# Kernel optimization log

Hardware: AMD Instinct MI355X
Metric: run time of the kernel (lower is better)

The kernel has to match this reference:

```python
import jax, jax.numpy as jnp
import numpy as np

NUM_LEVELS = 4
RADIUS = 4


def _avg_pool2(x):
    # x: [N, H, W] -> [N, H//2, W//2], 2x2 mean pool, stride 2 (F.avg_pool2d(corr,2,2))
    N, H, W = x.shape
    return x.reshape(N, H // 2, 2, W // 2, 2).mean(axis=(2, 4))


def _bilinear_sample(img, x, y):
    # img: [N, H, W]; x, y: [N, P] pixel coords.
    # Matches F.grid_sample(..., mode='bilinear', align_corners=True, padding_mode='zeros')
    # after the pixel->normalized->pixel round trip in bilinear_sampler (identity).
    N, H, W = img.shape
    x0 = jnp.floor(x)
    y0 = jnp.floor(y)
    wx = x - x0
    wy = y - y0
    x0i = x0.astype(jnp.int32)
    y0i = y0.astype(jnp.int32)
    flat = img.reshape(N, H * W)

    def gather(yi, xi):
        valid = (xi >= 0) & (xi <= W - 1) & (yi >= 0) & (yi <= H - 1)
        idx = jnp.clip(yi, 0, H - 1) * W + jnp.clip(xi, 0, W - 1)
        v = jnp.take_along_axis(flat, idx, axis=1)
        return jnp.where(valid, v, jnp.zeros((), img.dtype))

    v00 = gather(y0i, x0i)
    v01 = gather(y0i, x0i + 1)
    v10 = gather(y0i + 1, x0i)
    v11 = gather(y0i + 1, x0i + 1)
    return (v00 * (1 - wy) * (1 - wx) + v01 * (1 - wy) * wx
            + v10 * wy * (1 - wx) + v11 * wy * wx)


def _corr_block(fmap1, fmap2, coords):
    B, D, H, W = fmap1.shape
    # all-pairs correlation: [B, H*W, H*W] / sqrt(D)
    f1 = fmap1.reshape(B, D, H * W)
    f2 = fmap2.reshape(B, D, H * W)
    corr = jnp.einsum('bdn,bdm->bnm', f1, f2) / jnp.sqrt(jnp.asarray(D, fmap1.dtype))
    corr = corr.reshape(B * H * W, H, W)
    pyramid = [corr]
    for _ in range(NUM_LEVELS - 1):
        corr = _avg_pool2(corr)
        pyramid.append(corr)

    # coords: [B, 2, H, W] (x, y) -> [B*H*W, 2]
    c = coords.transpose(0, 2, 3, 1).reshape(B * H * W, 2)
    r = RADIUS
    d = jnp.linspace(-r, r, 2 * r + 1)
    dyg, dxg = jnp.meshgrid(d, d, indexing='ij')
    # faithful to torch: delta = stack(meshgrid(dy, dx), -1); channel 0 added to x, 1 to y
    delta = jnp.stack([dyg, dxg], axis=-1).reshape(-1, 2)  # [81, 2]

    outs = []
    for i, lvl in enumerate(pyramid):
        cl = c[:, None, :] / (2.0 ** i) + delta[None, :, :]  # [N, 81, 2]
        s = _bilinear_sample(lvl, cl[..., 0], cl[..., 1])    # [N, 81]
        outs.append(s.reshape(B, H, W, (2 * r + 1) ** 2))
    out = jnp.concatenate(outs, axis=-1)                     # [B, H, W, 4*81]
    return out.transpose(0, 3, 1, 2).astype(jnp.float32)


def setup_inputs() -> dict:
    key = jax.random.key(0)
    k1, k2, k3 = jax.random.split(key, 3)
    B, D, H, W = 2, 256, 80, 80
    fmap1 = jax.random.normal(k1, (B, D, H, W), dtype=jnp.float32)
    fmap2 = jax.random.normal(k2, (B, D, H, W), dtype=jnp.float32)
    # pixel coords in [0, W-1] x [0, H-1] (channel 0 = x, channel 1 = y)
    u = jax.random.uniform(k3, (B, 2, H, W), dtype=jnp.float32)
    scale = jnp.asarray([W - 1, H - 1], jnp.float32).reshape(1, 2, 1, 1)
    coords = u * scale
    return {"fmap1": fmap1, "fmap2": fmap2, "coords": coords}


def reference(fmap1, fmap2, coords):
    return _corr_block(fmap1, fmap2, coords)
```

## Files before the change

kernel.cpp:

```cpp
#include <hip/hip_runtime.h>


typedef _Float16 h2 __attribute__((ext_vector_type(2)));
typedef _Float16 half8 __attribute__((ext_vector_type(8)));
typedef float f32x4 __attribute__((ext_vector_type(4)));

#define HWDIM 80
#define DCH 256
#define NPIX 12800
#define NBUCKET 800

__global__ __launch_bounds__(256) void transpose_all(const float* __restrict__ f1,
                                                     const float* __restrict__ f2,
                                                     _Float16* __restrict__ f1h,
                                                     _Float16* __restrict__ f2p0) {
    __shared__ float tile[256][33];
    int bid = blockIdx.x;
    bool isf1 = bid < 400;
    int lb = isf1 ? bid : bid - 400;
    const float* src = isf1 ? f1 : f2;
    int b = lb / 200;
    int s0 = (lb % 200) * 32;
    int t = threadIdx.x;
    const float* sb = src + (size_t)b * DCH * (HWDIM * HWDIM);
#pragma unroll 4
    for (int k = 0; k < 32; ++k) {
        int j = t + 256 * k;
        int c = j >> 5, s = j & 31;
        tile[c][s] = sb[(size_t)c * (HWDIM * HWDIM) + s0 + s];
    }
    __syncthreads();
    int p = t & 127;
    int srow = t >> 7;
    if (isf1) {
        _Float16* db = f1h + ((size_t)b * 6400 + s0) * DCH;
#pragma unroll 4
        for (int k = 0; k < 16; ++k) {
            int s = 2 * k + srow;
            h2 v;
            v[0] = (_Float16)tile[2 * p][s];
            v[1] = (_Float16)tile[2 * p + 1][s];
            *(h2*)(db + (size_t)s * DCH + 2 * p) = v;
        }
    } else {
#pragma unroll 4
        for (int k = 0; k < 16; ++k) {
            int s = 2 * k + srow;
            int spatial = s0 + s;
            int yy = spatial / 80;
            int xx = spatial - yy * 80;
            h2 v;
            v[0] = (_Float16)tile[2 * p][s];
            v[1] = (_Float16)tile[2 * p + 1][s];
            size_t off = (size_t)b * 2073600 + (size_t)(p >> 4) * 259200
                       + ((size_t)(yy + 5) * 90 + (xx + 5)) * 32 + ((2 * p) & 31);
            *(h2*)(f2p0 + off) = v;
        }
    }
}

__global__ __launch_bounds__(256) void pool1(const _Float16* __restrict__ src,
                                             _Float16* __restrict__ dst) {
    int i = blockIdx.x * 256 + threadIdx.x;
    int c2 = i & 15;
    int r = i >> 4;
    int x = r % 40; r /= 40;
    int y = r % 40; r /= 40;
    int pl = r & 7;
    int b = r >> 3;
    const h2* s = (const h2*)src + ((size_t)b * 2073600 + (size_t)pl * 259200) / 2
                + ((size_t)(2 * y + 5) * 90 + (2 * x + 5)) * 16 + c2;
    h2 v00 = s[0], v01 = s[16], v10 = s[90 * 16], v11 = s[90 * 16 + 16];
    float r0 = ((float)v00[0] + (float)v01[0] + (float)v10[0] + (float)v11[0]) * 0.25f;
    float r1 = ((float)v00[1] + (float)v01[1] + (float)v10[1] + (float)v11[1]) * 0.25f;
    h2 o; o[0] = (_Float16)r0; o[1] = (_Float16)r1;
    *((h2*)dst + ((size_t)b * 640000 + (size_t)pl * 80000) / 2
      + ((size_t)(y + 5) * 50 + (x + 5)) * 16 + c2) = o;
}

__global__ __launch_bounds__(256) void pool23(const _Float16* __restrict__ l1,
                                              _Float16* __restrict__ l2,
                                              _Float16* __restrict__ l3) {
    int i = blockIdx.x * 256 + threadIdx.x;
    if (i < 102400) {
        int c2 = i & 15;
        int r = i >> 4;
        int x = r % 20; r /= 20;
        int y = r % 20; r /= 20;
        int pl = r & 7;
        int b = r >> 3;
        const h2* s = (const h2*)l1 + ((size_t)b * 640000 + (size_t)pl * 80000) / 2
                    + ((size_t)(2 * y + 5) * 50 + (2 * x + 5)) * 16 + c2;
        h2 v00 = s[0], v01 = s[16], v10 = s[50 * 16], v11 = s[50 * 16 + 16];
        float r0 = ((float)v00[0] + (float)v01[0] + (float)v10[0] + (float)v11[0]) * 0.25f;
        float r1 = ((float)v00[1] + (float)v01[1] + (float)v10[1] + (float)v11[1]) * 0.25f;
        h2 o; o[0] = (_Float16)r0; o[1] = (_Float16)r1;
        *((h2*)l2 + ((size_t)b * 230400 + (size_t)pl * 28800) / 2
          + ((size_t)(y + 5) * 30 + (x + 5)) * 16 + c2) = o;
    } else {
        int j = i - 102400;
        int c2 = j & 15;
        int r = j >> 4;
        int x = r % 10; r /= 10;
        int y = r % 10; r /= 10;
        int pl = r & 7;
        int b = r >> 3;
        const h2* s = (const h2*)l1 + ((size_t)b * 640000 + (size_t)pl * 80000) / 2 + c2;
        float r0 = 0.f, r1 = 0.f;
#pragma unroll
        for (int dy = 0; dy < 4; ++dy)
#pragma unroll
            for (int dx = 0; dx < 4; ++dx) {
                h2 v = s[((size_t)(4 * y + dy + 5) * 50 + (4 * x + dx + 5)) * 16];
                r0 += (float)v[0];
                r1 += (float)v[1];
            }
        h2 o; o[0] = (_Float16)(r0 * 0.0625f); o[1] = (_Float16)(r1 * 0.0625f);
        *((h2*)l3 + ((size_t)b * 102400 + (size_t)pl * 12800) / 2
          + ((size_t)(y + 5) * 20 + (x + 5)) * 16 + c2) = o;
    }
}

static __device__ __forceinline__ int bucket_of(const float* coords, int n) {
    int b = n / 6400;
    int r = n - b * 6400;
    float cx = coords[(size_t)b * 12800 + r];
    float cy = coords[(size_t)b * 12800 + 6400 + r];
    int ix = min(max((int)floorf(cx), 0), 79);
    int iy = min(max((int)floorf(cy), 0), 79);
    return b * 400 + (iy >> 2) * 20 + (ix >> 2);
}

__global__ __launch_bounds__(1024) void bucket_k(const float* __restrict__ coords,
                                                 int* __restrict__ sortedIdxP,
                                                 int* __restrict__ rank) {
    __shared__ unsigned int histS[NBUCKET], startS[NBUCKET], curS[NBUCKET];
    __shared__ unsigned int waveSum[16];
    int t = threadIdx.x;
    if (t < NBUCKET) histS[t] = 0u;
    __syncthreads();
    int bkt[13];
#pragma unroll
    for (int i = 0; i < 13; ++i) {
        int n = i * 1024 + t;
        if (n < NPIX) {
            bkt[i] = bucket_of(coords, n);
            atomicAdd(&histS[bkt[i]], 1u);
        }
    }
    __syncthreads();
    unsigned int v = (t < NBUCKET) ? ((histS[t] + 15u) & ~15u) : 0u;
    unsigned int x = v;
#pragma unroll
    for (int d = 1; d < 64; d <<= 1) {
        unsigned int y = __shfl_up(x, d);
        if ((t & 63) >= d) x += y;
    }
    if ((t & 63) == 63) waveSum[t >> 6] = x;
    __syncthreads();
    if (t < 16) {
        unsigned int w = waveSum[t];
#pragma unroll
        for (int d = 1; d < 16; d <<= 1) {
            unsigned int y = __shfl_up(w, d);
            if (t >= d) w += y;
        }
        waveSum[t] = w;
    }
    __syncthreads();
    unsigned int incl = x + ((t >> 6) ? waveSum[(t >> 6) - 1] : 0u);
    if (t < NBUCKET) {
        unsigned int e = incl - v;
        startS[t] = e;
        curS[t] = e;
    }
    __syncthreads();
#pragma unroll
    for (int i = 0; i < 13; ++i) {
        int n = i * 1024 + t;
        if (n < NPIX) {
            unsigned int pos = atomicAdd(&curS[bkt[i]], 1u);
            sortedIdxP[pos] = n;
            rank[n] = (int)pos;
        }
    }
    __syncthreads();
    if (t < NBUCKET) {
        unsigned int h = histS[t];
        if (h) {
            unsigned int pc = (h + 15u) & ~15u;
            unsigned int base = startS[t];
            int dup = sortedIdxP[base];
            for (unsigned int s = h; s < pc; ++s) sortedIdxP[base + s] = dup;
        }
    }
}

__global__ __launch_bounds__(512, 4) void corr_mfma(
    const _Float16* __restrict__ f1h,
    const _Float16* __restrict__ f2p0, const _Float16* __restrict__ f2p1,
    const _Float16* __restrict__ f2p2, const _Float16* __restrict__ f2p3,
    const float* __restrict__ coords, const int* __restrict__ sortedIdxP,
    _Float16* __restrict__ scratch) {
    __shared__ float G[528 * 17];
    __shared__ float fxS[4][16], fyS[4][16];
    __shared__ int lxS[4][16], lyS[4][16];
    __shared__ int X0cS[4], Y0cS[4], bS;

    int pphys = blockIdx.x;
    int l = (pphys & 7) * 200 + (pphys >> 3);
    int tid = threadIdx.x;
    if (sortedIdxP[l * 16] < 0) return;
    int lane = tid & 63;
    int wave = tid >> 6;

    int npx = sortedIdxP[l * 16 + (lane & 15)];
    const float4* f1p = (const float4*)(f1h + (size_t)npx * DCH);
    half8 bf[8];
#pragma unroll
    for (int kk = 0; kk < 8; ++kk)
        bf[kk] = __builtin_bit_cast(half8, f1p[(lane >> 4) + 4 * kk]);

    if (tid < 64) {
        int px = tid & 15, Lt = tid >> 4;
        int n = sortedIdxP[l * 16 + px];
        int b = n / 6400;
        int r = n - b * 6400;
        float cx = coords[(size_t)b * 12800 + r];
        float cy = coords[(size_t)b * 12800 + 6400 + r];
        float ls = 1.0f / (float)(1 << Lt);
        float cxl = cx * ls, cyl = cy * ls;
        float fxf = floorf(cxl), fyf = floorf(cyl);
        int X0 = (int)fxf - 4, Y0 = (int)fyf - 4;
        int ix = min(max((int)floorf(cx), 0), 79);
        int iy = min(max((int)floorf(cy), 0), 79);
        int X0c = (((ix >> 2) * 4) >> Lt) - 4;
        int Y0c = (((iy >> 2) * 4) >> Lt) - 4;
        lxS[Lt][px] = min(max(X0 - X0c, 0), 3);
        lyS[Lt][px] = min(max(Y0 - Y0c, 0), 3);
        fxS[Lt][px] = cxl - fxf;
        fyS[Lt][px] = cyl - fyf;
        X0cS[Lt] = X0c;
        Y0cS[Lt] = Y0c;
        if (tid == 0) bS = sortedIdxP[l * 16] / 6400;
    }
    __syncthreads();
    int b = bS;
    _Float16* sc = scratch + (size_t)l * 5184;

#pragma unroll
    for (int tt = 0; tt < 33; ++tt) {
        const int L  = tt < 11 ? 0 : tt < 19 ? 1 : tt < 26 ? 2 : 3;
        const int rt = tt - (L == 0 ? 0 : L == 1 ? 11 : L == 2 ? 19 : 26);
        const int Ww = L == 0 ? 13 : L == 1 ? 11 : 10;
        const int MT = L == 0 ? 169 : L == 1 ? 121 : 100;
        const int MAG = L == 0 ? 161320 : L == 1 ? 190652 : 209716;
        const int Wp = L == 0 ? 90 : L == 1 ? 50 : L == 2 ? 30 : 20;
        const int PS = L == 0 ? 259200 : L == 1 ? 80000 : L == 2 ? 28800 : 12800;
        const int PB = L == 0 ? 2073600 : L == 1 ? 640000 : L == 2 ? 230400 : 102400;
        const int GO = L == 0 ? 0 : L == 1 ? 176 : L == 2 ? 304 : 416;
        if (tt == 32 ? (wave != 7) : ((tt & 7) != wave)) continue;
        const _Float16* f2L = (L == 0 ? f2p0 : L == 1 ? f2p1 : L == 2 ? f2p2 : f2p3);
        const _Float16* f2b = f2L + (size_t)b * PB
                            + ((size_t)(Y0cS[L] + 5) * Wp + (X0cS[L] + 5)) * 32;
        int m = min(rt * 16 + (lane & 15), MT - 1);
        int my = (m * MAG) >> 21;
        int mx = m - my * Ww;
        const float4* ap = (const float4*)(f2b + (size_t)(my * Wp + mx) * 32)
                         + (lane >> 4);
        f32x4 acc = {0.f, 0.f, 0.f, 0.f};
#pragma unroll
        for (int kk = 0; kk < 8; ++kk) {
            half8 av = __builtin_bit_cast(half8, ap[kk * (PS / 8)]);
            acc = __builtin_amdgcn_mfma_f32_16x16x32_f16(av, bf[kk], acc, 0, 0, 0);
        }
        int gr = GO + rt * 16 + (lane >> 4) * 4;
#pragma unroll
        for (int r = 0; r < 4; ++r) G[(gr + r) * 17 + (lane & 15)] = acc[r];
    }
    __syncthreads();

    for (int idx = tid; idx < 5184; idx += 512) {
        int k2 = idx >> 4, x = idx & 15;
        int Le = (k2 * 810) >> 16;
        int k = k2 - Le * 81;
        int Ww = Le == 0 ? 13 : Le == 1 ? 11 : 10;
        int GO = Le == 0 ? 0 : Le == 1 ? 176 : Le == 2 ? 304 : 416;
        int a = (k * 57) >> 9;
        int c = k - 9 * a;
        int gx = lxS[Le][x] + a, gy = lyS[Le][x] + c;
        int m00 = GO + gy * Ww + gx;
        float fx = fxS[Le][x], fy = fyS[Le][x];
        float t00 = G[m00 * 17 + x];
        float t01 = G[(m00 + 1) * 17 + x];
        float t10 = G[(m00 + Ww) * 17 + x];
        float t11 = G[(m00 + Ww + 1) * 17 + x];
        float v = ((1.f - fy) * ((1.f - fx) * t00 + fx * t01)
                 + fy * ((1.f - fx) * t10 + fx * t11)) * 0.0625f;
        sc[idx] = (_Float16)v;
    }
}

__global__ __launch_bounds__(256) void unsort4(const _Float16* __restrict__ scratch,
                                               const int* __restrict__ rank,
                                               float* __restrict__ out) {
    int u = blockIdx.x * 256 + threadIdx.x;
    int q = u % 1600;
    int ch = (u / 1600) % 324;
    int b = u / (1600 * 324);
    int nl = q * 4;
    int4 rk = *(const int4*)(rank + b * 6400 + nl);
    float4 v;
    v.x = (float)scratch[(size_t)(rk.x >> 4) * 5184 + ch * 16 + (rk.x & 15)];
    v.y = (float)scratch[(size_t)(rk.y >> 4) * 5184 + ch * 16 + (rk.y & 15)];
    v.z = (float)scratch[(size_t)(rk.z >> 4) * 5184 + ch * 16 + (rk.z & 15)];
    v.w = (float)scratch[(size_t)(rk.w >> 4) * 5184 + ch * 16 + (rk.w & 15)];
    *(float4*)(out + ((size_t)b * 324 + ch) * 6400 + nl) = v;
}

extern "C" void kernel_launch(void* const* d_in, const int* in_sizes, int n_in,
                              void* d_out, int out_size, void* d_ws, size_t ws_size,
                              hipStream_t stream) {
    const float* fmap1 = (const float*)d_in[0];
    const float* fmap2 = (const float*)d_in[1];
    const float* coords = (const float*)d_in[2];
    float* out = (float*)d_out;
    char* ws = (char*)d_ws;

    _Float16* f1h  = (_Float16*)(ws);
    _Float16* f2p0 = (_Float16*)(ws + 6553600);
    _Float16* f2p1 = (_Float16*)(ws + 14848000);
    _Float16* f2p2 = (_Float16*)(ws + 17408000);
    _Float16* f2p3 = (_Float16*)(ws + 18329600);
    int* sortedIdxP = (int*)(ws + 18739200);
    int* rank       = (int*)(ws + 18841600);
    _Float16* scratch = (_Float16*)(ws + 18892800);

    hipMemsetAsync(f2p0, 0, 12185600, stream);
    hipMemsetAsync(sortedIdxP, 0xFF, 102400, stream);

    transpose_all<<<dim3(800), dim3(256), 0, stream>>>(fmap1, fmap2, f1h, f2p0);
    pool1<<<dim3(1600), dim3(256), 0, stream>>>(f2p0, f2p1);
    pool23<<<dim3(500), dim3(256), 0, stream>>>(f2p1, f2p2, f2p3);
    bucket_k<<<dim3(1), dim3(1024), 0, stream>>>(coords, sortedIdxP, rank);
    corr_mfma<<<dim3(1600), dim3(512), 0, stream>>>(f1h, f2p0, f2p1, f2p2, f2p3,
                                                    coords, sortedIdxP, scratch);
    unsort4<<<dim3(4050), dim3(256), 0, stream>>>(scratch, rank, out);
}
```

Measured before the change: 104.3 us.

## Fuse pooling kernels, drop memset, stage f1 in LDS, rebalance MFMA tiles

Merges the two pooling kernels into one launch that computes all three coarser levels directly from level 0, so later levels no longer wait on earlier ones. The memset of the sorted index buffer is removed; the bucket kernel now writes -1 into its unused tail. In the correlation kernel, f1 feature vectors are loaded once into LDS with coalesced loads, and the 33 tiles are split into contiguous compile-time ranges per wave. Launch bounds drop to 2 blocks, which frees registers but may reduce occupancy, and pooling straight from level 0 does more reads per output.

```diff
diff --git a/kernel.cpp b/kernel.cpp
--- a/kernel.cpp
+++ b/kernel.cpp
@@ -59,64 +59,67 @@
     }
 }
 
-__global__ __launch_bounds__(256) void pool1(const _Float16* __restrict__ src,
-                                             _Float16* __restrict__ dst) {
+__global__ __launch_bounds__(256) void pools(const _Float16* __restrict__ l0,
+                                             _Float16* __restrict__ l1,
+                                             _Float16* __restrict__ l2,
+                                             _Float16* __restrict__ l3) {
     int i = blockIdx.x * 256 + threadIdx.x;
-    int c2 = i & 15;
-    int r = i >> 4;
-    int x = r % 40; r /= 40;
-    int y = r % 40; r /= 40;
-    int pl = r & 7;
-    int b = r >> 3;
-    const h2* s = (const h2*)src + ((size_t)b * 2073600 + (size_t)pl * 259200) / 2
-                + ((size_t)(2 * y + 5) * 90 + (2 * x + 5)) * 16 + c2;
-    h2 v00 = s[0], v01 = s[16], v10 = s[90 * 16], v11 = s[90 * 16 + 16];
-    float r0 = ((float)v00[0] + (float)v01[0] + (float)v10[0] + (float)v11[0]) * 0.25f;
-    float r1 = ((float)v00[1] + (float)v01[1] + (float)v10[1] + (float)v11[1]) * 0.25f;
-    h2 o; o[0] = (_Float16)r0; o[1] = (_Float16)r1;
-    *((h2*)dst + ((size_t)b * 640000 + (size_t)pl * 80000) / 2
-      + ((size_t)(y + 5) * 50 + (x + 5)) * 16 + c2) = o;
-}
-
-__global__ __launch_bounds__(256) void pool23(const _Float16* __restrict__ l1,
-                                              _Float16* __restrict__ l2,
-                                              _Float16* __restrict__ l3) {
-    int i = blockIdx.x * 256 + threadIdx.x;
-    if (i < 102400) {
+    if (i < 409600) {
         int c2 = i & 15;
         int r = i >> 4;
+        int x = r % 40; r /= 40;
+        int y = r % 40; r /= 40;
+        int pl = r & 7;
+        int b = r >> 3;
+        const h2* s = (const h2*)l0 + (size_t)b * 1036800 + (size_t)pl * 129600
+                    + ((size_t)(2 * y + 5) * 90 + (2 * x + 5)) * 16 + c2;
+        h2 v00 = s[0], v01 = s[16], v10 = s[90 * 16], v11 = s[90 * 16 + 16];
+        float r0 = ((float)v00[0] + (float)v01[0] + (float)v10[0] + (float)v11[0]) * 0.25f;
+        float r1 = ((float)v00[1] + (float)v01[1] + (float)v10[1] + (float)v11[1]) * 0.25f;
+        h2 o; o[0] = (_Float16)r0; o[1] = (_Float16)r1;
+        *((h2*)l1 + (size_t)b * 320000 + (size_t)pl * 40000
+          + ((size_t)(y + 5) * 50 + (x + 5)) * 16 + c2) = o;
+    } else if (i < 512000) {
+        int j = i - 409600;
+        int c2 = j & 15;
+        int r = j >> 4;
         int x = r % 20; r /= 20;
         int y = r % 20; r /= 20;
         int pl = r & 7;
         int b = r >> 3;
-        const h2* s = (const h2*)l1 + ((size_t)b * 640000 + (size_t)pl * 80000) / 2
-                    + ((size_t)(2 * y + 5) * 50 + (2 * x + 5)) * 16 + c2;
-        h2 v00 = s[0], v01 = s[16], v10 = s[50 * 16], v11 = s[50 * 16 + 16];
-        float r0 = ((float)v00[0] + (float)v01[0] + (float)v10[0] + (float)v11[0]) * 0.25f;
-        float r1 = ((float)v00[1] + (float)v01[1] + (float)v10[1] + (float)v11[1]) * 0.25f;
-        h2 o; o[0] = (_Float16)r0; o[1] = (_Float16)r1;
-        *((h2*)l2 + ((size_t)b * 230400 + (size_t)pl * 28800) / 2
+        const h2* s = (const h2*)l0 + (size_t)b * 1036800 + (size_t)pl * 129600 + c2;
+        float r0 = 0.f, r1 = 0.f;
+#pragma unroll
+        for (int dy = 0; dy < 4; ++dy)
+#pragma unroll
+            for (int dx = 0; dx < 4; ++dx) {
+                h2 v = s[((size_t)(4 * y + dy + 5) * 90 + (4 * x + dx + 5)) * 16];
+                r0 += (float)v[0];
+                r1 += (float)v[1];
+            }
+        h2 o; o[0] = (_Float16)(r0 * 0.0625f); o[1] = (_Float16)(r1 * 0.0625f);
+        *((h2*)l2 + (size_t)b * 115200 + (size_t)pl * 14400
           + ((size_t)(y + 5) * 30 + (x + 5)) * 16 + c2) = o;
     } else {
-        int j = i - 102400;
+        int j = i - 512000;
         int c2 = j & 15;
         int r = j >> 4;
         int x = r % 10; r /= 10;
         int y = r % 10; r /= 10;
         int pl = r & 7;
         int b = r >> 3;
-        const h2* s = (const h2*)l1 + ((size_t)b * 640000 + (size_t)pl * 80000) / 2 + c2;
+        const h2* s = (const h2*)l0 + (size_t)b * 1036800 + (size_t)pl * 129600 + c2;
         float r0 = 0.f, r1 = 0.f;
 #pragma unroll
-        for (int dy = 0; dy < 4; ++dy)
-#pragma unroll
-            for (int dx = 0; dx < 4; ++dx) {
-                h2 v = s[((size_t)(4 * y + dy + 5) * 50 + (4 * x + dx + 5)) * 16];
+        for (int dy = 0; dy < 8; ++dy)
+#pragma unroll
+            for (int dx = 0; dx < 8; ++dx) {
+                h2 v = s[((size_t)(8 * y + dy + 5) * 90 + (8 * x + dx + 5)) * 16];
                 r0 += (float)v[0];
                 r1 += (float)v[1];
             }
-        h2 o; o[0] = (_Float16)(r0 * 0.0625f); o[1] = (_Float16)(r1 * 0.0625f);
-        *((h2*)l3 + ((size_t)b * 102400 + (size_t)pl * 12800) / 2
+        h2 o; o[0] = (_Float16)(r0 * 0.015625f); o[1] = (_Float16)(r1 * 0.015625f);
+        *((h2*)l3 + (size_t)b * 51200 + (size_t)pl * 6400
           + ((size_t)(y + 5) * 20 + (x + 5)) * 16 + c2) = o;
     }
 }
@@ -136,6 +139,7 @@
                                                  int* __restrict__ rank) {
     __shared__ unsigned int histS[NBUCKET], startS[NBUCKET], curS[NBUCKET];
     __shared__ unsigned int waveSum[16];
+    __shared__ unsigned int totalS;
     int t = threadIdx.x;
     if (t < NBUCKET) histS[t] = 0u;
     __syncthreads();
@@ -173,6 +177,7 @@
         unsigned int e = incl - v;
         startS[t] = e;
         curS[t] = e;
+        if (t == NBUCKET - 1) totalS = incl;
     }
     __syncthreads();
 #pragma unroll
@@ -194,15 +199,54 @@
             for (unsigned int s = h; s < pc; ++s) sortedIdxP[base + s] = dup;
         }
     }
-}
-
-__global__ __launch_bounds__(512, 4) void corr_mfma(
+    for (unsigned int s = totalS + t; s < 25600u; s += 1024u) sortedIdxP[s] = -1;
+}
+
+template <int TB, int TE>
+static __device__ __forceinline__ void run_tiles(
+    int lane, int b,
+    const _Float16* __restrict__ f2p0, const _Float16* __restrict__ f2p1,
+    const _Float16* __restrict__ f2p2, const _Float16* __restrict__ f2p3,
+    const int* X0cS, const int* Y0cS, const half8* bf, float* G) {
+#pragma unroll
+    for (int tt = TB; tt < TE; ++tt) {
+        const int L  = tt < 11 ? 0 : tt < 19 ? 1 : tt < 26 ? 2 : 3;
+        const int rt = tt - (L == 0 ? 0 : L == 1 ? 11 : L == 2 ? 19 : 26);
+        const int Ww = L == 0 ? 13 : L == 1 ? 11 : 10;
+        const int MT = L == 0 ? 169 : L == 1 ? 121 : 100;
+        const int MAG = L == 0 ? 161320 : L == 1 ? 190652 : 209716;
+        const int Wp = L == 0 ? 90 : L == 1 ? 50 : L == 2 ? 30 : 20;
+        const int PS = L == 0 ? 259200 : L == 1 ? 80000 : L == 2 ? 28800 : 12800;
+        const int PB = L == 0 ? 2073600 : L == 1 ? 640000 : L == 2 ? 230400 : 102400;
+        const int GO = L == 0 ? 0 : L == 1 ? 176 : L == 2 ? 304 : 416;
+        const _Float16* f2L = (L == 0 ? f2p0 : L == 1 ? f2p1 : L == 2 ? f2p2 : f2p3);
+        const _Float16* f2b = f2L + (size_t)b * PB
+                            + ((size_t)(Y0cS[L] + 5) * Wp + (X0cS[L] + 5)) * 32;
+        int m = min(rt * 16 + (lane & 15), MT - 1);
+        int my = (m * MAG) >> 21;
+        int mx = m - my * Ww;
+        const float4* ap = (const float4*)(f2b + (size_t)(my * Wp + mx) * 32)
+                         + (lane >> 4);
+        f32x4 acc = {0.f, 0.f, 0.f, 0.f};
+#pragma unroll
+        for (int kk = 0; kk < 8; ++kk) {
+            half8 av = __builtin_bit_cast(half8, ap[kk * (PS / 8)]);
+            acc = __builtin_amdgcn_mfma_f32_16x16x32_f16(av, bf[kk], acc, 0, 0, 0);
+        }
+        int gr = GO + rt * 16 + (lane >> 4) * 4;
+#pragma unroll
+        for (int r = 0; r < 4; ++r) G[(gr + r) * 17 + (lane & 15)] = acc[r];
+    }
+}
+
+__global__ __launch_bounds__(512, 2) void corr_mfma(
     const _Float16* __restrict__ f1h,
     const _Float16* __restrict__ f2p0, const _Float16* __restrict__ f2p1,
     const _Float16* __restrict__ f2p2, const _Float16* __restrict__ f2p3,
     const float* __restrict__ coords, const int* __restrict__ sortedIdxP,
     _Float16* __restrict__ scratch) {
     __shared__ float G[528 * 17];
+    __shared__ _Float16 f1S[16 * 264];
     __shared__ float fxS[4][16], fyS[4][16];
     __shared__ int lxS[4][16], lyS[4][16];
     __shared__ int X0cS[4], Y0cS[4], bS;
@@ -214,13 +258,12 @@
     int lane = tid & 63;
     int wave = tid >> 6;
 
-    int npx = sortedIdxP[l * 16 + (lane & 15)];
-    const float4* f1p = (const float4*)(f1h + (size_t)npx * DCH);
-    half8 bf[8];
-#pragma unroll
-    for (int kk = 0; kk < 8; ++kk)
-        bf[kk] = __builtin_bit_cast(half8, f1p[(lane >> 4) + 4 * kk]);
-
+    {
+        int px = tid >> 5, q = tid & 31;
+        int n = sortedIdxP[l * 16 + px];
+        const float4* src = (const float4*)(f1h + (size_t)n * DCH);
+        *((float4*)(f1S + px * 264) + q) = src[q];
+    }
     if (tid < 64) {
         int px = tid & 15, Lt = tid >> 4;
         int n = sortedIdxP[l * 16 + px];
@@ -246,40 +289,23 @@
     }
     __syncthreads();
     int b = bS;
+
+    half8 bf[8];
+#pragma unroll
+    for (int kk = 0; kk < 8; ++kk)
+        bf[kk] = *(const half8*)(f1S + (lane & 15) * 264 + ((lane >> 4) + 4 * kk) * 8);
+
+    if      (wave == 0) run_tiles<0, 5>(lane, b, f2p0, f2p1, f2p2, f2p3, X0cS, Y0cS, bf, G);
+    else if (wave == 1) run_tiles<5, 9>(lane, b, f2p0, f2p1, f2p2, f2p3, X0cS, Y0cS, bf, G);
+    else if (wave == 2) run_tiles<9, 13>(lane, b, f2p0, f2p1, f2p2, f2p3, X0cS, Y0cS, bf, G);
+    else if (wave == 3) run_tiles<13, 17>(lane, b, f2p0, f2p1, f2p2, f2p3, X0cS, Y0cS, bf, G);
+    else if (wave == 4) run_tiles<17, 21>(lane, b, f2p0, f2p1, f2p2, f2p3, X0cS, Y0cS, bf, G);
+    else if (wave == 5) run_tiles<21, 25>(lane, b, f2p0, f2p1, f2p2, f2p3, X0cS, Y0cS, bf, G);
+    else if (wave == 6) run_tiles<25, 29>(lane, b, f2p0, f2p1, f2p2, f2p3, X0cS, Y0cS, bf, G);
+    else                run_tiles<29, 33>(lane, b, f2p0, f2p1, f2p2, f2p3, X0cS, Y0cS, bf, G);
+    __syncthreads();
+
     _Float16* sc = scratch + (size_t)l * 5184;
-
-#pragma unroll
-    for (int tt = 0; tt < 33; ++tt) {
-        const int L  = tt < 11 ? 0 : tt < 19 ? 1 : tt < 26 ? 2 : 3;
-        const int rt = tt - (L == 0 ? 0 : L == 1 ? 11 : L == 2 ? 19 : 26);
-        const int Ww = L == 0 ? 13 : L == 1 ? 11 : 10;
-        const int MT = L == 0 ? 169 : L == 1 ? 121 : 100;
-        const int MAG = L == 0 ? 161320 : L == 1 ? 190652 : 209716;
-        const int Wp = L == 0 ? 90 : L == 1 ? 50 : L == 2 ? 30 : 20;
-        const int PS = L == 0 ? 259200 : L == 1 ? 80000 : L == 2 ? 28800 : 12800;
-        const int PB = L == 0 ? 2073600 : L == 1 ? 640000 : L == 2 ? 230400 : 102400;
-        const int GO = L == 0 ? 0 : L == 1 ? 176 : L == 2 ? 304 : 416;
-        if (tt == 32 ? (wave != 7) : ((tt & 7) != wave)) continue;
-        const _Float16* f2L = (L == 0 ? f2p0 : L == 1 ? f2p1 : L == 2 ? f2p2 : f2p3);
-        const _Float16* f2b = f2L + (size_t)b * PB
-                            + ((size_t)(Y0cS[L] + 5) * Wp + (X0cS[L] + 5)) * 32;
-        int m = min(rt * 16 + (lane & 15), MT - 1);
-        int my = (m * MAG) >> 21;
-        int mx = m - my * Ww;
-        const float4* ap = (const float4*)(f2b + (size_t)(my * Wp + mx) * 32)
-                         + (lane >> 4);
-        f32x4 acc = {0.f, 0.f, 0.f, 0.f};
-#pragma unroll
-        for (int kk = 0; kk < 8; ++kk) {
-            half8 av = __builtin_bit_cast(half8, ap[kk * (PS / 8)]);
-            acc = __builtin_amdgcn_mfma_f32_16x16x32_f16(av, bf[kk], acc, 0, 0, 0);
-        }
-        int gr = GO + rt * 16 + (lane >> 4) * 4;
-#pragma unroll
-        for (int r = 0; r < 4; ++r) G[(gr + r) * 17 + (lane & 15)] = acc[r];
-    }
-    __syncthreads();
-
     for (int idx = tid; idx < 5184; idx += 512) {
         int k2 = idx >> 4, x = idx & 15;
         int Le = (k2 * 810) >> 16;
@@ -337,11 +363,9 @@
     _Float16* scratch = (_Float16*)(ws + 18892800);
 
     hipMemsetAsync(f2p0, 0, 12185600, stream);
-    hipMemsetAsync(sortedIdxP, 0xFF, 102400, stream);
 
     transpose_all<<<dim3(800), dim3(256), 0, stream>>>(fmap1, fmap2, f1h, f2p0);
-    pool1<<<dim3(1600), dim3(256), 0, stream>>>(f2p0, f2p1);
-    pool23<<<dim3(500), dim3(256), 0, stream>>>(f2p1, f2p2, f2p3);
+    pools<<<dim3(2100), dim3(256), 0, stream>>>(f2p0, f2p1, f2p2, f2p3);
     bucket_k<<<dim3(1), dim3(1024), 0, stream>>>(coords, sortedIdxP, rank);
     corr_mfma<<<dim3(1600), dim3(512), 0, stream>>>(f1h, f2p0, f2p1, f2p2, f2p3,
                                                     coords, sortedIdxP, scratch);
```

After: 97.90 us. -6.1%, faster.
